# Kernel tuning notes

Hardware: AMD Instinct MI355X
Metric: run time of the kernel (lower is better)

The kernel has to match this reference:

```python
import jax, jax.numpy as jnp
import numpy as np

N = 50000      # nodes
E = 800000     # edges (avg degree 16)
D_IN, D_H, D_OUT = 128, 128, 64
EPS = 1e-5


def setup_inputs() -> dict:
    key = jax.random.key(0)
    ks = jax.random.split(key, 6)
    feat = jax.random.normal(ks[0], (N, D_IN), dtype=jnp.float32)
    # Consistent CSR adjacency: sorted destination rows -> nodePointer via searchsorted
    rows = np.sort(np.asarray(jax.random.randint(ks[1], (E,), 0, N, dtype=jnp.int32)))
    edge_rows = jnp.asarray(rows, dtype=jnp.int32)              # [E] destination node per edge
    nodePointer = jnp.asarray(np.searchsorted(rows, np.arange(N + 1)), dtype=jnp.int32)  # [N+1]
    edgeList = jax.random.randint(ks[2], (E,), 0, N, dtype=jnp.int32)  # [E] source (column) indices
    def glorot(k, i, o):
        return jax.random.normal(k, (i, o), dtype=jnp.float32) * (1.0 / np.sqrt(i)).astype(np.float32)
    W0 = glorot(ks[3], D_IN, D_H)
    W1 = glorot(ks[4], D_H, D_H)
    W2 = glorot(ks[5], D_H, D_OUT)
    return {"feat": feat, "W0": W0, "W1": W1, "W2": W2,
            "nodePointer": nodePointer, "edgeList": edgeList, "edge_rows": edge_rows}


def _layer_norm(x):
    # Fresh nn.LayerNorm each forward in the original => weight=1, bias=0
    mu = jnp.mean(x, axis=-1, keepdims=True)
    var = jnp.mean(jnp.square(x - mu), axis=-1, keepdims=True)
    return (x - mu) * jax.lax.rsqrt(var + EPS)


def reference(feat, W0, W1, W2, nodePointer, edgeList, edge_rows):
    h = feat
    Ws = [W0, W1, W2]
    n_layers = len(Ws)
    for l, W in enumerate(Ws):
        xw = h @ W                      # [N, d_out] dense GEMM
        msg = xw[edgeList]              # [E, d_out] gather source-node features
        h = jax.ops.segment_sum(msg, edge_rows, num_segments=N)  # SpMM: A @ (h W)
        h = _layer_norm(h)
        if l != n_layers - 1:
            h = jax.nn.relu(h)
    return h
```

## Files before the change

kernel.cpp:

```cpp
#include <hip/hip_runtime.h>
#include <cstddef>


typedef __attribute__((ext_vector_type(8))) short bf16x8;
typedef __attribute__((ext_vector_type(4))) float floatx4;
typedef __attribute__((ext_vector_type(4))) unsigned int uintx4;
typedef __attribute__((ext_vector_type(2))) unsigned int uintx2;

static __device__ __forceinline__ unsigned int f2bf(float f) {
    union { float f; unsigned int u; } v; v.f = f;
    unsigned int u = v.u;
    u += 0x7fffu + ((u >> 16) & 1u);
    return u >> 16;
}
static __device__ __forceinline__ float bf_lo(unsigned int p) {
    union { unsigned int u; float f; } v; v.u = p << 16; return v.f;
}
static __device__ __forceinline__ float bf_hi(unsigned int p) {
    union { unsigned int u; float f; } v; v.u = p & 0xffff0000u; return v.f;
}
static __device__ __forceinline__ void acc8(float* a, uintx4 v) {
    a[0] += bf_lo(v.x); a[1] += bf_hi(v.x);
    a[2] += bf_lo(v.y); a[3] += bf_hi(v.y);
    a[4] += bf_lo(v.z); a[5] += bf_hi(v.z);
    a[6] += bf_lo(v.w); a[7] += bf_hi(v.w);
}
static __device__ __forceinline__ void acc4(float* a, uintx2 v) {
    a[0] += bf_lo(v.x); a[1] += bf_hi(v.x);
    a[2] += bf_lo(v.y); a[3] += bf_hi(v.y);
}

__global__ __launch_bounds__(256) void cvt_w(const float* __restrict__ W0,
                                             const float* __restrict__ W1,
                                             const float* __restrict__ W2,
                                             unsigned int* __restrict__ WtF) {
    const int m = blockIdx.x >> 4;
    const int slice = blockIdx.x & 15;
    const float* W = (m == 0) ? W0 : (m == 1) ? W1 : W2;
    const int ncols = (m == 2) ? 64 : 128;
    unsigned int* dst = WtF + m * 128 * 64;
    const int total = ncols * 64;
    for (int idx = slice * 256 + threadIdx.x; idx < total; idx += 16 * 256) {
        const int j    = idx & 3;
        const int lane = (idx >> 2) & 63;
        const int s    = (idx >> 8) & 3;
        const int t    = idx >> 10;
        const int mcol = lane & 15;
        const int quad = lane >> 4;
        const int n = t * 16 + mcol;
        const int k = s * 32 + quad * 8 + 2 * j;
        unsigned int lo = f2bf(W[(size_t)k * ncols + n]);
        unsigned int hi = f2bf(W[(size_t)(k + 1) * ncols + n]);
        dst[idx] = (hi << 16) | lo;
    }
}

template <int NCOLS, bool A_FP32>
__global__ __launch_bounds__(64) void gemm_mfma(const void* __restrict__ Av,
                                                const unsigned int* __restrict__ Wt,
                                                unsigned int* __restrict__ C,
                                                int M) {
    const int lane = threadIdx.x;
    const int row0 = blockIdx.x * 16;
    const int quad = lane >> 4;
    const int mcol = lane & 15;

    constexpr int NT = NCOLS / 16;
    floatx4 acc[NT];
    #pragma unroll
    for (int t = 0; t < NT; ++t) acc[t] = (floatx4){0.f, 0.f, 0.f, 0.f};

    int aidx = row0 + mcol; if (aidx >= M) aidx = M - 1;
    const float*        arowF = (const float*)Av + (size_t)aidx * 128 + quad * 8;
    const unsigned int* afrag = (const unsigned int*)Av + (size_t)blockIdx.x * 1024 + lane * 4;
    const unsigned int* bbase = Wt + lane * 4;

    #pragma unroll
    for (int s = 0; s < 4; ++s) {
        bf16x8 a;
        if constexpr (A_FP32) {
            float4 fa = *(const float4*)(arowF + s * 32);
            float4 fb = *(const float4*)(arowF + s * 32 + 4);
            uintx4 ap;
            ap.x = (f2bf(fa.y) << 16) | f2bf(fa.x);
            ap.y = (f2bf(fa.w) << 16) | f2bf(fa.z);
            ap.z = (f2bf(fb.y) << 16) | f2bf(fb.x);
            ap.w = (f2bf(fb.w) << 16) | f2bf(fb.z);
            a = __builtin_bit_cast(bf16x8, ap);
        } else {
            uintx4 ap = *(const uintx4*)(afrag + s * 256);
            a = __builtin_bit_cast(bf16x8, ap);
        }
        #pragma unroll
        for (int t = 0; t < NT; ++t) {
            uintx4 bp = *(const uintx4*)(bbase + t * 1024 + s * 256);
            bf16x8 b = __builtin_bit_cast(bf16x8, bp);
            acc[t] = __builtin_amdgcn_mfma_f32_16x16x32_bf16(a, b, acc[t], 0, 0, 0);
        }
    }

    const int rowStride = NCOLS >> 1;
    #pragma unroll
    for (int t = 0; t < NT; ++t) {
        #pragma unroll
        for (int r = 0; r < 4; ++r) {
            unsigned int mybf = f2bf(acc[t][r]);
            unsigned int pair = __shfl_xor(mybf, 1, 64);
            int orow = row0 + quad * 4 + r;
            if (orow < M && (mcol & 1) == 0) {
                unsigned int packed = (pair << 16) | mybf;
                C[(size_t)orow * rowStride + t * 8 + (mcol >> 1)] = packed;
            }
        }
    }
}

template <int NCOLS_OUT>
__global__ __launch_bounds__(256) void agg_gemm(const unsigned int* __restrict__ xw,
                                                const int* __restrict__ ptr,
                                                const int* __restrict__ col,
                                                const unsigned int* __restrict__ Wt,
                                                unsigned int* __restrict__ C,
                                                int N) {
    __shared__ unsigned int lds[1024];
    const int tile = blockIdx.x;
    const int wave = threadIdx.x >> 6;
    const int lane = threadIdx.x & 63;
    const int g  = lane >> 4;
    const int sl = lane & 15;

    const unsigned int* base = xw + sl * 4;
    #pragma unroll
    for (int n = 0; n < 4; ++n) {
        const int m = wave * 4 + n;
        const int node = tile * 16 + m;
        const int nodeC = node < N ? node : N - 1;
        const int s = ptr[nodeC];
        const int e = node < N ? ptr[nodeC + 1] : s;

        float accA[8] = {}, accB[8] = {};
        int i = s + g;
        for (; i + 12 < e; i += 16) {
            uintx4 v0 = *(const uintx4*)(base + (size_t)col[i]      * 64);
            uintx4 v1 = *(const uintx4*)(base + (size_t)col[i + 4]  * 64);
            uintx4 v2 = *(const uintx4*)(base + (size_t)col[i + 8]  * 64);
            uintx4 v3 = *(const uintx4*)(base + (size_t)col[i + 12] * 64);
            acc8(accA, v0); acc8(accB, v1); acc8(accA, v2); acc8(accB, v3);
        }
        for (; i < e; i += 4) {
            uintx4 v0 = *(const uintx4*)(base + (size_t)col[i] * 64);
            acc8(accA, v0);
        }

        float acc[8];
        #pragma unroll
        for (int j = 0; j < 8; ++j) acc[j] = accA[j] + accB[j];

        #pragma unroll
        for (int j = 0; j < 8; ++j) {
            acc[j] += __shfl_xor(acc[j], 16, 64);
            acc[j] += __shfl_xor(acc[j], 32, 64);
        }
        float s1 = 0.f, s2 = 0.f;
        #pragma unroll
        for (int j = 0; j < 8; ++j) { s1 += acc[j]; s2 += acc[j] * acc[j]; }
        #pragma unroll
        for (int mm = 8; mm >= 1; mm >>= 1) {
            s1 += __shfl_xor(s1, mm, 64);
            s2 += __shfl_xor(s2, mm, 64);
        }
        const float mean = s1 * (1.0f / 128.0f);
        const float var  = s2 * (1.0f / 128.0f) - mean * mean;
        const float inv  = rsqrtf(var + 1e-5f);

        if (g == 0) {
            float o[8];
            #pragma unroll
            for (int j = 0; j < 8; ++j)
                o[j] = fmaxf((acc[j] - mean) * inv, 0.f);
            uintx4 p;
            p.x = (f2bf(o[1]) << 16) | f2bf(o[0]);
            p.y = (f2bf(o[3]) << 16) | f2bf(o[2]);
            p.z = (f2bf(o[5]) << 16) | f2bf(o[4]);
            p.w = (f2bf(o[7]) << 16) | f2bf(o[6]);
            *(uintx4*)(lds + (sl >> 2) * 256 + (sl & 3) * 64 + m * 4) = p;
        }
    }
    __syncthreads();

    constexpr int WT = NCOLS_OUT / 64;
    const int quad = lane >> 4;
    const int mcol = lane & 15;
    floatx4 acc[WT];
    #pragma unroll
    for (int t = 0; t < WT; ++t) acc[t] = (floatx4){0.f, 0.f, 0.f, 0.f};

    const unsigned int* bbase = Wt + lane * 4;
    #pragma unroll
    for (int s4 = 0; s4 < 4; ++s4) {
        uintx4 ap = *(const uintx4*)(lds + s4 * 256 + lane * 4);
        bf16x8 a = __builtin_bit_cast(bf16x8, ap);
        #pragma unroll
        for (int tt = 0; tt < WT; ++tt) {
            const int t = wave * WT + tt;
            uintx4 bp = *(const uintx4*)(bbase + t * 1024 + s4 * 256);
            bf16x8 b = __builtin_bit_cast(bf16x8, bp);
            acc[tt] = __builtin_amdgcn_mfma_f32_16x16x32_bf16(a, b, acc[tt], 0, 0, 0);
        }
    }

    const int rowStride = NCOLS_OUT >> 1;
    #pragma unroll
    for (int tt = 0; tt < WT; ++tt) {
        const int t = wave * WT + tt;
        #pragma unroll
        for (int r = 0; r < 4; ++r) {
            unsigned int mybf = f2bf(acc[tt][r]);
            unsigned int pair = __shfl_xor(mybf, 1, 64);
            const int orow = tile * 16 + quad * 4 + r;
            if (orow < N && (mcol & 1) == 0) {
                unsigned int packed = (pair << 16) | mybf;
                C[(size_t)orow * rowStride + t * 8 + (mcol >> 1)] = packed;
            }
        }
    }
}

__global__ __launch_bounds__(256) void agg_ln64(const unsigned int* __restrict__ xw,
                                                const int* __restrict__ ptr,
                                                const int* __restrict__ col,
                                                float* __restrict__ out, int N) {
    const int node = blockIdx.x * 4 + (threadIdx.x >> 6);
    if (node >= N) return;
    const int lane = threadIdx.x & 63;
    const int g  = lane >> 4;
    const int sl = lane & 15;
    const int s = ptr[node];
    const int e = ptr[node + 1];

    float accA[4] = {}, accB[4] = {};
    const unsigned int* base = xw + sl * 2;
    int i = s + g;
    for (; i + 12 < e; i += 16) {
        uintx2 v0 = *(const uintx2*)(base + (size_t)col[i]      * 32);
        uintx2 v1 = *(const uintx2*)(base + (size_t)col[i + 4]  * 32);
        uintx2 v2 = *(const uintx2*)(base + (size_t)col[i + 8]  * 32);
        uintx2 v3 = *(const uintx2*)(base + (size_t)col[i + 12] * 32);
        acc4(accA, v0); acc4(accB, v1); acc4(accA, v2); acc4(accB, v3);
    }
    for (; i < e; i += 4) {
        uintx2 v0 = *(const uintx2*)(base + (size_t)col[i] * 32);
        acc4(accA, v0);
    }

    float acc[4];
    #pragma unroll
    for (int j = 0; j < 4; ++j) acc[j] = accA[j] + accB[j];

    #pragma unroll
    for (int j = 0; j < 4; ++j) {
        acc[j] += __shfl_xor(acc[j], 16, 64);
        acc[j] += __shfl_xor(acc[j], 32, 64);
    }
    float s1 = 0.f, s2 = 0.f;
    #pragma unroll
    for (int j = 0; j < 4; ++j) { s1 += acc[j]; s2 += acc[j] * acc[j]; }
    #pragma unroll
    for (int m = 8; m >= 1; m >>= 1) {
        s1 += __shfl_xor(s1, m, 64);
        s2 += __shfl_xor(s2, m, 64);
    }
    const float mean = s1 * (1.0f / 64.0f);
    const float var  = s2 * (1.0f / 64.0f) - mean * mean;
    const float inv  = rsqrtf(var + 1e-5f);

    if (g == 0) {
        float4 o;
        o.x = (acc[0] - mean) * inv;
        o.y = (acc[1] - mean) * inv;
        o.z = (acc[2] - mean) * inv;
        o.w = (acc[3] - mean) * inv;
        *(float4*)(out + (size_t)node * 64 + sl * 4) = o;
    }
}

extern "C" void kernel_launch(void* const* d_in, const int* in_sizes, int n_in,
                              void* d_out, int out_size, void* d_ws, size_t ws_size,
                              hipStream_t stream) {
    const float* feat = (const float*)d_in[0];
    const float* W0   = (const float*)d_in[1];
    const float* W1   = (const float*)d_in[2];
    const float* W2   = (const float*)d_in[3];
    const int*   ptr  = (const int*)d_in[4];
    const int*   col  = (const int*)d_in[5];

    const int N = in_sizes[4] - 1;

    unsigned int* buf0 = (unsigned int*)d_ws;
    unsigned int* buf1 = buf0 + (size_t)N * 64;
    unsigned int* WtP  = buf1 + (size_t)N * 64;
    float*        out  = (float*)d_out;

    const int gemmBlocks = (N + 15) / 16;
    const int nodeBlocks = (N + 3) / 4;

    cvt_w<<<48, 256, 0, stream>>>(W0, W1, W2, WtP);

    gemm_mfma<128, true><<<gemmBlocks, 64, 0, stream>>>(feat, WtP, buf0, N);
    agg_gemm<128><<<gemmBlocks, 256, 0, stream>>>(buf0, ptr, col, WtP + 128 * 64, buf1, N);
    agg_gemm<64><<<gemmBlocks, 256, 0, stream>>>(buf1, ptr, col, WtP + 2 * 128 * 64, buf0, N);
    agg_ln64<<<nodeBlocks, 256, 0, stream>>>(buf0, ptr, col, out, N);
}
```

Before: 198.6 us.

## Interleave four nodes' gathers per wave with software-pipelined column/feature loads

The aggregation loops in agg_gemm and agg_ln64 now process all four nodes of a wave together. Column indices are prefetched two rounds ahead and feature gathers one round ahead, so more independent memory loads are in flight per wave. agg_ln64 now handles 16 nodes per block like agg_gemm, and edge indices are clamped to stay in bounds. The cost is predicated, wasted loads for nodes whose degree is below the wave's maximum, plus higher register pressure from holding four accumulators and the prefetch buffers.

```diff
diff --git a/kernel.cpp b/kernel.cpp
--- a/kernel.cpp
+++ b/kernel.cpp
@@ -121,7 +121,7 @@
                                                 const int* __restrict__ col,
                                                 const unsigned int* __restrict__ Wt,
                                                 unsigned int* __restrict__ C,
-                                                int N) {
+                                                int N, int Emax ) {
     __shared__ unsigned int lds[1024];
     const int tile = blockIdx.x;
     const int wave = threadIdx.x >> 6;
@@ -129,41 +129,77 @@
     const int g  = lane >> 4;
     const int sl = lane & 15;
 
+    int s0[4], len[4];
+    int maxlen = 0;
+    #pragma unroll
+    for (int n = 0; n < 4; ++n) {
+        const int node = tile * 16 + wave * 4 + n;
+        const int nc = node < N ? node : N - 1;
+        const int a = ptr[nc];
+        const int b = node < N ? ptr[nc + 1] : a;
+        s0[n] = a; len[n] = b - a;
+        maxlen = max(maxlen, len[n]);
+    }
+
+    float acc[4][8] = {};
     const unsigned int* base = xw + sl * 4;
+
+    if (maxlen > 0) {
+        #define LOADCOL(dst, OFF)                                            \
+            _Pragma("unroll")                                                \
+            for (int n = 0; n < 4; ++n) {                                    \
+                int idx = (OFF) + g;                                         \
+                idx = idx < len[n] ? idx : 0;                                \
+                int ei = s0[n] + idx;                                        \
+                ei = ei < Emax ? ei : Emax;                                  \
+                dst[n] = col[ei];                                            \
+            }
+        #define GATHER4(dst, c)                                              \
+            _Pragma("unroll")                                                \
+            for (int n = 0; n < 4; ++n)                                      \
+                dst[n] = *(const uintx4*)(base + (size_t)c[n] * 64);
+        #define ACCUM4(v, OFF)                                               \
+            _Pragma("unroll")                                                \
+            for (int n = 0; n < 4; ++n)                                      \
+                if ((OFF) + g < len[n]) acc8(acc[n], v[n]);
+
+        int cA[4], cB[4], cC[4], cD[4];
+        uintx4 vA[4], vB[4];
+        LOADCOL(cA, 0)
+        LOADCOL(cB, 4)
+        GATHER4(vA, cA)
+        LOADCOL(cC, 8)
+        GATHER4(vB, cB)
+        LOADCOL(cD, 12)
+
+        const int rounds = (maxlen + 7) & ~7;
+        for (int off = 0; off < rounds; off += 8) {
+            ACCUM4(vA, off)
+            GATHER4(vA, cC)
+            LOADCOL(cC, off + 16)
+            ACCUM4(vB, off + 4)
+            GATHER4(vB, cD)
+            LOADCOL(cD, off + 20)
+        }
+        #undef LOADCOL
+        #undef GATHER4
+        #undef ACCUM4
+    }
+
     #pragma unroll
     for (int n = 0; n < 4; ++n) {
         const int m = wave * 4 + n;
-        const int node = tile * 16 + m;
-        const int nodeC = node < N ? node : N - 1;
-        const int s = ptr[nodeC];
-        const int e = node < N ? ptr[nodeC + 1] : s;
-
-        float accA[8] = {}, accB[8] = {};
-        int i = s + g;
-        for (; i + 12 < e; i += 16) {
-            uintx4 v0 = *(const uintx4*)(base + (size_t)col[i]      * 64);
-            uintx4 v1 = *(const uintx4*)(base + (size_t)col[i + 4]  * 64);
-            uintx4 v2 = *(const uintx4*)(base + (size_t)col[i + 8]  * 64);
-            uintx4 v3 = *(const uintx4*)(base + (size_t)col[i + 12] * 64);
-            acc8(accA, v0); acc8(accB, v1); acc8(accA, v2); acc8(accB, v3);
-        }
-        for (; i < e; i += 4) {
-            uintx4 v0 = *(const uintx4*)(base + (size_t)col[i] * 64);
-            acc8(accA, v0);
-        }
-
-        float acc[8];
-        #pragma unroll
-        for (int j = 0; j < 8; ++j) acc[j] = accA[j] + accB[j];
-
+        float a8[8];
         #pragma unroll
         for (int j = 0; j < 8; ++j) {
-            acc[j] += __shfl_xor(acc[j], 16, 64);
-            acc[j] += __shfl_xor(acc[j], 32, 64);
+            float t = acc[n][j];
+            t += __shfl_xor(t, 16, 64);
+            t += __shfl_xor(t, 32, 64);
+            a8[j] = t;
         }
         float s1 = 0.f, s2 = 0.f;
         #pragma unroll
-        for (int j = 0; j < 8; ++j) { s1 += acc[j]; s2 += acc[j] * acc[j]; }
+        for (int j = 0; j < 8; ++j) { s1 += a8[j]; s2 += a8[j] * a8[j]; }
         #pragma unroll
         for (int mm = 8; mm >= 1; mm >>= 1) {
             s1 += __shfl_xor(s1, mm, 64);
@@ -177,7 +213,7 @@
             float o[8];
             #pragma unroll
             for (int j = 0; j < 8; ++j)
-                o[j] = fmaxf((acc[j] - mean) * inv, 0.f);
+                o[j] = fmaxf((a8[j] - mean) * inv, 0.f);
             uintx4 p;
             p.x = (f2bf(o[1]) << 16) | f2bf(o[0]);
             p.y = (f2bf(o[3]) << 16) | f2bf(o[2]);
@@ -191,9 +227,9 @@
     constexpr int WT = NCOLS_OUT / 64;
     const int quad = lane >> 4;
     const int mcol = lane & 15;
-    floatx4 acc[WT];
-    #pragma unroll
-    for (int t = 0; t < WT; ++t) acc[t] = (floatx4){0.f, 0.f, 0.f, 0.f};
+    floatx4 macc[WT];
+    #pragma unroll
+    for (int t = 0; t < WT; ++t) macc[t] = (floatx4){0.f, 0.f, 0.f, 0.f};
 
     const unsigned int* bbase = Wt + lane * 4;
     #pragma unroll
@@ -205,7 +241,7 @@
             const int t = wave * WT + tt;
             uintx4 bp = *(const uintx4*)(bbase + t * 1024 + s4 * 256);
             bf16x8 b = __builtin_bit_cast(bf16x8, bp);
-            acc[tt] = __builtin_amdgcn_mfma_f32_16x16x32_bf16(a, b, acc[tt], 0, 0, 0);
+            macc[tt] = __builtin_amdgcn_mfma_f32_16x16x32_bf16(a, b, macc[tt], 0, 0, 0);
         }
     }
 
@@ -215,7 +251,7 @@
         const int t = wave * WT + tt;
         #pragma unroll
         for (int r = 0; r < 4; ++r) {
-            unsigned int mybf = f2bf(acc[tt][r]);
+            unsigned int mybf = f2bf(macc[tt][r]);
             unsigned int pair = __shfl_xor(mybf, 1, 64);
             const int orow = tile * 16 + quad * 4 + r;
             if (orow < N && (mcol & 1) == 0) {
@@ -229,58 +265,102 @@
 __global__ __launch_bounds__(256) void agg_ln64(const unsigned int* __restrict__ xw,
                                                 const int* __restrict__ ptr,
                                                 const int* __restrict__ col,
-                                                float* __restrict__ out, int N) {
-    const int node = blockIdx.x * 4 + (threadIdx.x >> 6);
-    if (node >= N) return;
+                                                float* __restrict__ out,
+                                                int N, int Emax) {
+    const int tile = blockIdx.x;
+    const int wave = threadIdx.x >> 6;
     const int lane = threadIdx.x & 63;
     const int g  = lane >> 4;
     const int sl = lane & 15;
-    const int s = ptr[node];
-    const int e = ptr[node + 1];
-
-    float accA[4] = {}, accB[4] = {};
+
+    int s0[4], len[4];
+    int maxlen = 0;
+    #pragma unroll
+    for (int n = 0; n < 4; ++n) {
+        const int node = tile * 16 + wave * 4 + n;
+        const int nc = node < N ? node : N - 1;
+        const int a = ptr[nc];
+        const int b = node < N ? ptr[nc + 1] : a;
+        s0[n] = a; len[n] = b - a;
+        maxlen = max(maxlen, len[n]);
+    }
+
+    float acc[4][4] = {};
     const unsigned int* base = xw + sl * 2;
-    int i = s + g;
-    for (; i + 12 < e; i += 16) {
-        uintx2 v0 = *(const uintx2*)(base + (size_t)col[i]      * 32);
-        uintx2 v1 = *(const uintx2*)(base + (size_t)col[i + 4]  * 32);
-        uintx2 v2 = *(const uintx2*)(base + (size_t)col[i + 8]  * 32);
-        uintx2 v3 = *(const uintx2*)(base + (size_t)col[i + 12] * 32);
-        acc4(accA, v0); acc4(accB, v1); acc4(accA, v2); acc4(accB, v3);
-    }
-    for (; i < e; i += 4) {
-        uintx2 v0 = *(const uintx2*)(base + (size_t)col[i] * 32);
-        acc4(accA, v0);
-    }
-
-    float acc[4];
-    #pragma unroll
-    for (int j = 0; j < 4; ++j) acc[j] = accA[j] + accB[j];
-
-    #pragma unroll
-    for (int j = 0; j < 4; ++j) {
-        acc[j] += __shfl_xor(acc[j], 16, 64);
-        acc[j] += __shfl_xor(acc[j], 32, 64);
-    }
-    float s1 = 0.f, s2 = 0.f;
-    #pragma unroll
-    for (int j = 0; j < 4; ++j) { s1 += acc[j]; s2 += acc[j] * acc[j]; }
-    #pragma unroll
-    for (int m = 8; m >= 1; m >>= 1) {
-        s1 += __shfl_xor(s1, m, 64);
-        s2 += __shfl_xor(s2, m, 64);
-    }
-    const float mean = s1 * (1.0f / 64.0f);
-    const float var  = s2 * (1.0f / 64.0f) - mean * mean;
-    const float inv  = rsqrtf(var + 1e-5f);
-
-    if (g == 0) {
-        float4 o;
-        o.x = (acc[0] - mean) * inv;
-        o.y = (acc[1] - mean) * inv;
-        o.z = (acc[2] - mean) * inv;
-        o.w = (acc[3] - mean) * inv;
-        *(float4*)(out + (size_t)node * 64 + sl * 4) = o;
+
+    if (maxlen > 0) {
+        #define LOADCOL(dst, OFF)                                            \
+            _Pragma("unroll")                                                \
+            for (int n = 0; n < 4; ++n) {                                    \
+                int idx = (OFF) + g;                                         \
+                idx = idx < len[n] ? idx : 0;                                \
+                int ei = s0[n] + idx;                                        \
+                ei = ei < Emax ? ei : Emax;                                  \
+                dst[n] = col[ei];                                            \
+            }
+        #define GATHER2(dst, c)                                              \
+            _Pragma("unroll")                                                \
+            for (int n = 0; n < 4; ++n)                                      \
+                dst[n] = *(const uintx2*)(base + (size_t)c[n] * 32);
+        #define ACCUM2(v, OFF)                                               \
+            _Pragma("unroll")                                                \
+            for (int n = 0; n < 4; ++n)                                      \
+                if ((OFF) + g < len[n]) acc4(acc[n], v[n]);
+
+        int cA[4], cB[4], cC[4], cD[4];
+        uintx2 vA[4], vB[4];
+        LOADCOL(cA, 0)
+        LOADCOL(cB, 4)
+        GATHER2(vA, cA)
+        LOADCOL(cC, 8)
+        GATHER2(vB, cB)
+        LOADCOL(cD, 12)
+
+        const int rounds = (maxlen + 7) & ~7;
+        for (int off = 0; off < rounds; off += 8) {
+            ACCUM2(vA, off)
+            GATHER2(vA, cC)
+            LOADCOL(cC, off + 16)
+            ACCUM2(vB, off + 4)
+            GATHER2(vB, cD)
+            LOADCOL(cD, off + 20)
+        }
+        #undef LOADCOL
+        #undef GATHER2
+        #undef ACCUM2
+    }
+
+    #pragma unroll
+    for (int n = 0; n < 4; ++n) {
+        const int node = tile * 16 + wave * 4 + n;
+        float a4[4];
+        #pragma unroll
+        for (int j = 0; j < 4; ++j) {
+            float t = acc[n][j];
+            t += __shfl_xor(t, 16, 64);
+            t += __shfl_xor(t, 32, 64);
+            a4[j] = t;
+        }
+        float s1 = 0.f, s2 = 0.f;
+        #pragma unroll
+        for (int j = 0; j < 4; ++j) { s1 += a4[j]; s2 += a4[j] * a4[j]; }
+        #pragma unroll
+        for (int mm = 8; mm >= 1; mm >>= 1) {
+            s1 += __shfl_xor(s1, mm, 64);
+            s2 += __shfl_xor(s2, mm, 64);
+        }
+        const float mean = s1 * (1.0f / 64.0f);
+        const float var  = s2 * (1.0f / 64.0f) - mean * mean;
+        const float inv  = rsqrtf(var + 1e-5f);
+
+        if (g == 0 && node < N) {
+            float4 o;
+            o.x = (a4[0] - mean) * inv;
+            o.y = (a4[1] - mean) * inv;
+            o.z = (a4[2] - mean) * inv;
+            o.w = (a4[3] - mean) * inv;
+            *(float4*)(out + (size_t)node * 64 + sl * 4) = o;
+        }
     }
 }
 
@@ -295,19 +375,20 @@
     const int*   col  = (const int*)d_in[5];
 
     const int N = in_sizes[4] - 1;
+    const int E = in_sizes[5];
+    const int Emax = E - 1;
 
     unsigned int* buf0 = (unsigned int*)d_ws;
     unsigned int* buf1 = buf0 + (size_t)N * 64;
     unsigned int* WtP  = buf1 + (size_t)N * 64;
     float*        out  = (float*)d_out;
 
-    const int gemmBlocks = (N + 15) / 16;
-    const int nodeBlocks = (N + 3) / 4;
+    const int tileBlocks = (N + 15) / 16;
 
     cvt_w<<<48, 256, 0, stream>>>(W0, W1, W2, WtP);
 
-    gemm_mfma<128, true><<<gemmBlocks, 64, 0, stream>>>(feat, WtP, buf0, N);
-    agg_gemm<128><<<gemmBlocks, 256, 0, stream>>>(buf0, ptr, col, WtP + 128 * 64, buf1, N);
-    agg_gemm<64><<<gemmBlocks, 256, 0, stream>>>(buf1, ptr, col, WtP + 2 * 128 * 64, buf0, N);
-    agg_ln64<<<nodeBlocks, 256, 0, stream>>>(buf0, ptr, col, out, N);
-}
+    gemm_mfma<128, true><<<tileBlocks, 64, 0, stream>>>(feat, WtP, buf0, N);
+    agg_gemm<128><<<tileBlocks, 256, 0, stream>>>(buf0, ptr, col, WtP + 128 * 64, buf1, N, Emax);
+    agg_gemm<64><<<tileBlocks, 256, 0, stream>>>(buf1, ptr, col, WtP + 2 * 128 * 64, buf0, N, Emax);
+    agg_ln64<<<tileBlocks, 256, 0, stream>>>(buf0, ptr, col, out, N, Emax);
+}
```

Result: faster. 189.0 us (-4.9%).
